# Performance work log

Measured on AMD Instinct MI355X. Metric: run time of the kernel, lower is better.

Reference implementation:

```python
import jax, jax.numpy as jnp
import numpy as np

N = 50000   # nodes
E = 800000  # edges
D = 128     # feature width (in_feats == hidden dims)
LN_EPS = 1e-5


def _degrees(src, dst, n):
    ones = jnp.ones(src.shape[0], dtype=jnp.float32)
    deg_out = jax.ops.segment_sum(ones, src, num_segments=n)
    deg_in = jax.ops.segment_sum(ones, dst, num_segments=n)
    # DGL norm='both' clamps degrees to min 1
    return jnp.maximum(deg_out, 1.0), jnp.maximum(deg_in, 1.0)


def _graph_conv(h, src, dst, inv_sqrt_out, inv_sqrt_in, W, b):
    # DGL GraphConv, norm='both': D^{-1/2} A^T D^{-1/2} X W + b
    h = h * inv_sqrt_out[:, None]                       # pre-normalize by src out-degree
    msgs = h[src]                                       # [E, D] gather
    agg = jax.ops.segment_sum(msgs, dst, num_segments=N)  # scatter-add to dst
    agg = agg * inv_sqrt_in[:, None]                    # post-normalize by dst in-degree
    return agg @ W + b


def _layer_norm(x, gamma, beta):
    mu = jnp.mean(x, axis=-1, keepdims=True)
    var = jnp.mean((x - mu) ** 2, axis=-1, keepdims=True)
    return (x - mu) * jax.lax.rsqrt(var + LN_EPS) * gamma + beta


def setup_inputs() -> dict:
    key = jax.random.key(0)
    ks = jax.random.split(key, 8)
    features = jax.random.normal(ks[0], (N, D), dtype=jnp.float32)
    src = jax.random.randint(ks[1], (E,), 0, N, dtype=jnp.int64)
    dst = jax.random.randint(ks[2], (E,), 0, N, dtype=jnp.int64)
    scale = 1.0 / np.sqrt(D)
    W1 = jax.random.normal(ks[3], (D, D), dtype=jnp.float32) * scale
    b1 = jnp.zeros((D,), dtype=jnp.float32)
    g1 = jnp.ones((D,), dtype=jnp.float32)
    be1 = jnp.zeros((D,), dtype=jnp.float32)
    W2 = jax.random.normal(ks[4], (D, D), dtype=jnp.float32) * scale
    b2 = jnp.zeros((D,), dtype=jnp.float32)
    g2 = jnp.ones((D,), dtype=jnp.float32)
    be2 = jnp.zeros((D,), dtype=jnp.float32)
    return {"features": features, "src": src, "dst": dst,
            "W1": W1, "b1": b1, "g1": g1, "be1": be1,
            "W2": W2, "b2": b2, "g2": g2, "be2": be2}


def reference(features, src, dst, W1, b1, g1, be1, W2, b2, g2, be2):
    deg_out, deg_in = _degrees(src, dst, N)
    iso = jax.lax.rsqrt(deg_out)
    isi = jax.lax.rsqrt(deg_in)
    # layer 1: GraphConv -> LayerNorm -> ReLU (dropout p=0, eval mode)
    h = _graph_conv(features, src, dst, iso, isi, W1, b1)
    h = jax.nn.relu(_layer_norm(h, g1, be1))
    # layer 2
    h = _graph_conv(h, src, dst, iso, isi, W2, b2)
    h = jax.nn.relu(_layer_norm(h, g2, be2))
    return h
```

## Files before the change

### kernel.cpp

```cpp
#include <hip/hip_runtime.h>
#include <stdint.h>

#define NN 50000
#define DD 128
#define EE 800000
#define LN_EPS 1e-5f
#define SCAN_BLOCKS ((NN + 255) / 256)
#define ROWS 16
#define ASTRIDE 136

#define CH 256
#define EC (EE / CH)
#define NP8 50000
#define NW (NP8 / 4)

typedef __attribute__((ext_vector_type(8))) short bf8_t;
typedef __attribute__((ext_vector_type(4))) float f32x4;

static __device__ __forceinline__ unsigned short f2bf(float f) {
    unsigned u = __float_as_uint(f);
    u += 0x7FFFu + ((u >> 16) & 1u);
    return (unsigned short)(u >> 16);
}

#define BF16ACC(u) do { \
    acc[0] += __uint_as_float((u).x << 16); \
    acc[1] += __uint_as_float((u).x & 0xffff0000u); \
    acc[2] += __uint_as_float((u).y << 16); \
    acc[3] += __uint_as_float((u).y & 0xffff0000u); \
    acc[4] += __uint_as_float((u).z << 16); \
    acc[5] += __uint_as_float((u).z & 0xffff0000u); \
    acc[6] += __uint_as_float((u).w << 16); \
    acc[7] += __uint_as_float((u).w & 0xffff0000u); \
} while (0)

__global__ __launch_bounds__(256) void hist_kernel(
    const int* __restrict__ src, const int* __restrict__ dst,
    unsigned char* __restrict__ epos8,
    unsigned int* __restrict__ histI, unsigned int* __restrict__ histO) {
    __shared__ unsigned int lh[NW];
    int tid = threadIdx.x;
    int c = blockIdx.x;
    int e0 = c * EC, e1 = e0 + EC;

    for (int w = tid; w < NW; w += 256) lh[w] = 0;
    __syncthreads();
    for (int e = e0 + tid; e < e1; e += 256) {
        int d = dst[e];
        int f = (d & 3) * 8;
        unsigned old = atomicAdd(&lh[d >> 2], 1u << f);
        epos8[e] = (unsigned char)(old >> f);
    }
    __syncthreads();
    {
        unsigned int* o = histI + (size_t)c * NW;
        for (int w = tid; w < NW; w += 256) o[w] = lh[w];
    }
    __syncthreads();

    for (int w = tid; w < NW; w += 256) lh[w] = 0;
    __syncthreads();
    for (int e = e0 + tid; e < e1; e += 256) {
        int d = src[e];
        atomicAdd(&lh[d >> 2], 1u << ((d & 3) * 8));
    }
    __syncthreads();
    {
        unsigned int* o = histO + (size_t)c * NW;
        for (int w = tid; w < NW; w += 256) o[w] = lh[w];
    }
}

__global__ __launch_bounds__(256) void sum_kernel(
    unsigned char* __restrict__ histI8,
    const unsigned char* __restrict__ histO8,
    int* __restrict__ cntI, float* __restrict__ iso, float* __restrict__ isi,
    int* __restrict__ bsum) {
    __shared__ int s[256];
    int tid = threadIdx.x;
    int n = blockIdx.x * 256 + tid;

    int ci = 0, co = 0;
    if (n < NN) {
#pragma unroll 8
        for (int c = 0; c < CH; c++) {
            size_t idx = (size_t)c * NP8 + n;
            unsigned char v = histI8[idx];
            histI8[idx] = (unsigned char)ci;
            ci += v;
            co += histO8[idx];
        }
        iso[n] = rsqrtf(fmaxf((float)co, 1.0f));
        isi[n] = rsqrtf(fmaxf((float)ci, 1.0f));
        cntI[n] = ci;
    }
    s[tid] = (n < NN) ? ci : 0;
    __syncthreads();
    for (int off = 128; off > 0; off >>= 1) {
        if (tid < off) s[tid] += s[tid + off];
        __syncthreads();
    }
    if (tid == 0) bsum[blockIdx.x] = s[0];
}

__global__ __launch_bounds__(256) void scanC_kernel(
    const int* __restrict__ cnt, const int* __restrict__ bsum,
    int* __restrict__ rowptr,
    const float* __restrict__ feat, const float* __restrict__ iso,
    unsigned short* __restrict__ hb) {
    __shared__ int s[256];
    __shared__ int base_s;
    __shared__ float iso_s[256];
    int tid = threadIdx.x;
    int i = blockIdx.x * 256 + tid;

    int bv = (tid < SCAN_BLOCKS && tid < blockIdx.x) ? bsum[tid] : 0;
    s[tid] = bv;
    __syncthreads();
    for (int off = 128; off > 0; off >>= 1) {
        if (tid < off) s[tid] += s[tid + off];
        __syncthreads();
    }
    if (tid == 0) base_s = s[0];
    __syncthreads();
    int base = base_s;

    iso_s[tid] = (i < NN) ? iso[i] : 1.f;
    __syncthreads();

    int v = (i < NN) ? cnt[i] : 0;
    s[tid] = v;
    __syncthreads();
    for (int off = 1; off < 256; off <<= 1) {
        int t = (tid >= off) ? s[tid - off] : 0;
        __syncthreads();
        s[tid] += t;
        __syncthreads();
    }
    if (i < NN) rowptr[i] = base + s[tid] - v;
    if (blockIdx.x == 0 && tid == 0) rowptr[NN] = EE;

    int rr = tid >> 5;
    int q = tid & 31;
    int row0 = blockIdx.x * 256;
#pragma unroll 4
    for (int it = 0; it < 32; it++) {
        int r = it * 8 + rr;
        int row = row0 + r;
        if (row < NN) {
            float sc = iso_s[r];
            float4 fv = ((const float4*)feat)[(size_t)row * 32 + q];
            ushort4 o;
            o.x = f2bf(fv.x * sc); o.y = f2bf(fv.y * sc);
            o.z = f2bf(fv.z * sc); o.w = f2bf(fv.w * sc);
            ((ushort4*)hb)[(size_t)row * 32 + q] = o;
        }
    }
}

__global__ void fill_kernel(const int* __restrict__ src, const int* __restrict__ dst,
                            const unsigned char* __restrict__ epos8,
                            const unsigned char* __restrict__ choff8,
                            const int* __restrict__ rowptr, int* __restrict__ csr,
                            const float* __restrict__ W1, const float* __restrict__ W2,
                            unsigned short* __restrict__ wbt1, unsigned short* __restrict__ wbt2) {
    int e = blockIdx.x * blockDim.x + threadIdx.x;
    if (e < EE) {
        int d = dst[e];
        int c = e / EC;
        int pos = rowptr[d] + (int)choff8[(size_t)c * NP8 + d] + (int)epos8[e];
        csr[pos] = src[e];
    }
    if (blockIdx.x < 128) {
        int idx = (blockIdx.x & 63) * 256 + threadIdx.x;
        const float* W = (blockIdx.x < 64) ? W1 : W2;
        unsigned short* wt = (blockIdx.x < 64) ? wbt1 : wbt2;
        int k = idx >> 7, n = idx & 127;
        wt[n * 128 + k] = f2bf(W[idx]);
    }
}

template <int OUTMODE>
__global__ __launch_bounds__(256) void fused_layer(
    const unsigned short* __restrict__ hb, const int* __restrict__ csr,
    const int* __restrict__ rowptr, const float* __restrict__ isi,
    const float* __restrict__ iso,
    const unsigned short* __restrict__ wbt, const float* __restrict__ b,
    const float* __restrict__ g, const float* __restrict__ be,
    float* __restrict__ outf, unsigned short* __restrict__ outb) {
    __shared__ unsigned short Asb[ROWS][ASTRIDE];
    __shared__ float redS[4][16], redSS[4][16];

    int tid = threadIdx.x;
    int node0 = blockIdx.x * ROWS;
    int w = tid >> 6;
    int lane = tid & 63;
    int quad = lane >> 4;
    int l = lane & 15;

    {
        int r = tid >> 4;
        int n = node0 + r;
        float acc[8];
#pragma unroll
        for (int i = 0; i < 8; i++) acc[i] = 0.f;
        int beg = rowptr[n];
        int end = rowptr[n + 1];
        int j = beg;
        for (; j + 7 < end; j += 8) {
            int s0 = csr[j];     int s1 = csr[j + 1];
            int s2 = csr[j + 2]; int s3 = csr[j + 3];
            int s4 = csr[j + 4]; int s5 = csr[j + 5];
            int s6 = csr[j + 6]; int s7 = csr[j + 7];
            uint4 u0 = ((const uint4*)(hb + (size_t)s0 * DD))[l];
            uint4 u1 = ((const uint4*)(hb + (size_t)s1 * DD))[l];
            uint4 u2 = ((const uint4*)(hb + (size_t)s2 * DD))[l];
            uint4 u3 = ((const uint4*)(hb + (size_t)s3 * DD))[l];
            uint4 u4 = ((const uint4*)(hb + (size_t)s4 * DD))[l];
            uint4 u5 = ((const uint4*)(hb + (size_t)s5 * DD))[l];
            uint4 u6 = ((const uint4*)(hb + (size_t)s6 * DD))[l];
            uint4 u7 = ((const uint4*)(hb + (size_t)s7 * DD))[l];
            BF16ACC(u0); BF16ACC(u1); BF16ACC(u2); BF16ACC(u3);
            BF16ACC(u4); BF16ACC(u5); BF16ACC(u6); BF16ACC(u7);
        }
        for (; j < end; j++) {
            int s0 = csr[j];
            uint4 u0 = ((const uint4*)(hb + (size_t)s0 * DD))[l];
            BF16ACC(u0);
        }
        uint4 pk;
        pk.x = (unsigned)f2bf(acc[0]) | ((unsigned)f2bf(acc[1]) << 16);
        pk.y = (unsigned)f2bf(acc[2]) | ((unsigned)f2bf(acc[3]) << 16);
        pk.z = (unsigned)f2bf(acc[4]) | ((unsigned)f2bf(acc[5]) << 16);
        pk.w = (unsigned)f2bf(acc[6]) | ((unsigned)f2bf(acc[7]) << 16);
        *(uint4*)&Asb[r][l * 8] = pk;
    }
    __syncthreads();

    bf8_t af[4];
#pragma unroll
    for (int kb = 0; kb < 4; kb++)
        af[kb] = *(bf8_t*)&Asb[l][kb * 32 + quad * 8];

    f32x4 acc[2];
#pragma unroll
    for (int tc = 0; tc < 2; tc++) acc[tc] = (f32x4){0.f, 0.f, 0.f, 0.f};

#pragma unroll
    for (int tc = 0; tc < 2; tc++) {
        int n = w * 32 + tc * 16 + l;
#pragma unroll
        for (int kb = 0; kb < 4; kb++) {
            bf8_t bfr = *(const bf8_t*)&wbt[(size_t)n * 128 + kb * 32 + quad * 8];
            acc[tc] = __builtin_amdgcn_mfma_f32_16x16x32_bf16(af[kb], bfr, acc[tc], 0, 0, 0);
        }
    }

    float bb[2], ggv[2], bev[2];
    int cbase = w * 32 + l;
#pragma unroll
    for (int tc = 0; tc < 2; tc++) {
        int c = cbase + tc * 16;
        bb[tc] = b[c]; ggv[tc] = g[c]; bev[tc] = be[c];
    }

    float s[4], ss[4];
#pragma unroll
    for (int i = 0; i < 4; i++) {
        int n = node0 + quad * 4 + i;
        float isin = isi[n];
        s[i] = 0.f; ss[i] = 0.f;
#pragma unroll
        for (int tc = 0; tc < 2; tc++) {
            float v = acc[tc][i] * isin + bb[tc];
            acc[tc][i] = v;
            s[i] += v; ss[i] += v * v;
        }
    }
#pragma unroll
    for (int i = 0; i < 4; i++) {
#pragma unroll
        for (int m = 1; m <= 8; m <<= 1) {
            s[i] += __shfl_xor(s[i], m);
            ss[i] += __shfl_xor(ss[i], m);
        }
    }
    if (l == 0) {
#pragma unroll
        for (int i = 0; i < 4; i++) {
            redS[w][quad * 4 + i] = s[i];
            redSS[w][quad * 4 + i] = ss[i];
        }
    }
    __syncthreads();

#pragma unroll
    for (int i = 0; i < 4; i++) {
        int r = quad * 4 + i;
        float S  = redS[0][r] + redS[1][r] + redS[2][r] + redS[3][r];
        float SS = redSS[0][r] + redSS[1][r] + redSS[2][r] + redSS[3][r];
        float mu = S * (1.f / 128.f);
        float var = SS * (1.f / 128.f) - mu * mu;
        float rstd = rsqrtf(var + LN_EPS);
        int n = node0 + r;
        float isov = (OUTMODE == 1) ? iso[n] : 0.f;
        size_t base = (size_t)n * DD;
#pragma unroll
        for (int tc = 0; tc < 2; tc++) {
            float o = fmaxf((acc[tc][i] - mu) * rstd * ggv[tc] + bev[tc], 0.f);
            int c = cbase + tc * 16;
            if (OUTMODE == 0) {
                outf[base + c] = o;
            } else {
                outb[base + c] = f2bf(o * isov);
            }
        }
    }
}

static inline char* alignp(char* p, size_t a) {
    return (char*)(((uintptr_t)p + a - 1) & ~(uintptr_t)(a - 1));
}

extern "C" void kernel_launch(void* const* d_in, const int* in_sizes, int n_in,
                              void* d_out, int out_size, void* d_ws, size_t ws_size,
                              hipStream_t stream) {
    const float* features = (const float*)d_in[0];
    const int*   src      = (const int*)d_in[1];
    const int*   dst      = (const int*)d_in[2];
    const float* W1  = (const float*)d_in[3];
    const float* b1  = (const float*)d_in[4];
    const float* g1  = (const float*)d_in[5];
    const float* be1 = (const float*)d_in[6];
    const float* W2  = (const float*)d_in[7];
    const float* b2  = (const float*)d_in[8];
    const float* g2  = (const float*)d_in[9];
    const float* be2 = (const float*)d_in[10];
    float* out = (float*)d_out;

    char* p = (char*)d_ws;
    int* cntI = (int*)p;                 p = alignp(p + NN * 4, 256);
    int* rowptr = (int*)p;               p = alignp(p + (NN + 1) * 4, 256);
    int* bsum = (int*)p;                 p = alignp(p + SCAN_BLOCKS * 4, 256);
    int* csr = (int*)p;                  p = alignp(p + (size_t)EE * 4, 256);
    float* iso = (float*)p;              p = alignp(p + NN * 4, 256);
    float* isi = (float*)p;              p = alignp(p + NN * 4, 256);
    unsigned short* hb1 = (unsigned short*)p;  p = alignp(p + (size_t)NN * DD * 2, 256);
    unsigned short* hb2 = (unsigned short*)p;  p = alignp(p + (size_t)NN * DD * 2, 256);
    unsigned short* wbt1 = (unsigned short*)p; p = alignp(p + DD * DD * 2, 256);
    unsigned short* wbt2 = (unsigned short*)p; p = alignp(p + DD * DD * 2, 256);
    unsigned char* epos8 = (unsigned char*)p;  p = alignp(p + EE, 256);

    unsigned char* histI8 = (unsigned char*)hb2;
    unsigned char* histO8 = (unsigned char*)hb1;

    hist_kernel<<<CH, 256, 0, stream>>>(src, dst, epos8,
                                        (unsigned int*)histI8, (unsigned int*)histO8);
    sum_kernel<<<SCAN_BLOCKS, 256, 0, stream>>>(histI8, histO8, cntI, iso, isi, bsum);
    scanC_kernel<<<SCAN_BLOCKS, 256, 0, stream>>>(cntI, bsum, rowptr, features, iso, hb1);
    fill_kernel<<<(EE + 255) / 256, 256, 0, stream>>>(src, dst, epos8, histI8,
                                                      rowptr, csr, W1, W2, wbt1, wbt2);

    const int fblocks = NN / ROWS;
    fused_layer<1><<<fblocks, 256, 0, stream>>>(hb1, csr, rowptr, isi, iso,
                                                wbt1, b1, g1, be1, nullptr, hb2);
    fused_layer<0><<<fblocks, 256, 0, stream>>>(hb2, csr, rowptr, isi, iso,
                                                wbt2, b2, g2, be2, out, nullptr);
}
```

Measured before the change: 255.3 us.

## Fuse degree histograms, recompute edge slots in fill, and predicate gather tail

The histogram kernel now builds the in-degree and out-degree shared-memory histograms in a single pass over the edges, using two LDS arrays, and no longer writes per-edge slot bytes. The fill kernel now runs one block per edge chunk. It loads that chunk's offsets into LDS and recomputes each edge's slot with LDS atomics, which removes the epos8 buffer and its global round trip. The aggregation loop in the fused layer replaces the unrolled-by-8 loop plus scalar tail with a single masked loop that clamps indices, so short rows issue duplicate loads. Risks: per-block LDS use becomes large (about 100KB in the histogram kernel), fill parallelism drops to 256 blocks, and CSR order within a row becomes nondeterministic.

After: 232.9 us. 1.1x faster.

```diff
diff --git a/kernel.cpp b/kernel.cpp
--- a/kernel.cpp
+++ b/kernel.cpp
@@ -36,38 +36,26 @@
 
 __global__ __launch_bounds__(256) void hist_kernel(
     const int* __restrict__ src, const int* __restrict__ dst,
-    unsigned char* __restrict__ epos8,
     unsigned int* __restrict__ histI, unsigned int* __restrict__ histO) {
-    __shared__ unsigned int lh[NW];
+    __shared__ unsigned int lhI[NW];
+    __shared__ unsigned int lhO[NW];
     int tid = threadIdx.x;
     int c = blockIdx.x;
     int e0 = c * EC, e1 = e0 + EC;
 
-    for (int w = tid; w < NW; w += 256) lh[w] = 0;
+    for (int w = tid; w < NW; w += 256) { lhI[w] = 0; lhO[w] = 0; }
     __syncthreads();
     for (int e = e0 + tid; e < e1; e += 256) {
         int d = dst[e];
-        int f = (d & 3) * 8;
-        unsigned old = atomicAdd(&lh[d >> 2], 1u << f);
-        epos8[e] = (unsigned char)(old >> f);
+        int s = src[e];
+        atomicAdd(&lhI[d >> 2], 1u << ((d & 3) * 8));
+        atomicAdd(&lhO[s >> 2], 1u << ((s & 3) * 8));
     }
     __syncthreads();
     {
-        unsigned int* o = histI + (size_t)c * NW;
-        for (int w = tid; w < NW; w += 256) o[w] = lh[w];
-    }
-    __syncthreads();
-
-    for (int w = tid; w < NW; w += 256) lh[w] = 0;
-    __syncthreads();
-    for (int e = e0 + tid; e < e1; e += 256) {
-        int d = src[e];
-        atomicAdd(&lh[d >> 2], 1u << ((d & 3) * 8));
-    }
-    __syncthreads();
-    {
-        unsigned int* o = histO + (size_t)c * NW;
-        for (int w = tid; w < NW; w += 256) o[w] = lh[w];
+        unsigned int* oi = histI + (size_t)c * NW;
+        unsigned int* oo = histO + (size_t)c * NW;
+        for (int w = tid; w < NW; w += 256) { oi[w] = lhI[w]; oo[w] = lhO[w]; }
     }
 }
 
@@ -158,23 +146,34 @@
     }
 }
 
-__global__ void fill_kernel(const int* __restrict__ src, const int* __restrict__ dst,
-                            const unsigned char* __restrict__ epos8,
-                            const unsigned char* __restrict__ choff8,
-                            const int* __restrict__ rowptr, int* __restrict__ csr,
-                            const float* __restrict__ W1, const float* __restrict__ W2,
-                            unsigned short* __restrict__ wbt1, unsigned short* __restrict__ wbt2) {
-    int e = blockIdx.x * blockDim.x + threadIdx.x;
-    if (e < EE) {
+__global__ __launch_bounds__(256) void fill_kernel(
+    const int* __restrict__ src, const int* __restrict__ dst,
+    const unsigned char* __restrict__ choff8,
+    const int* __restrict__ rowptr, int* __restrict__ csr,
+    const float* __restrict__ W1, const float* __restrict__ W2,
+    unsigned short* __restrict__ wbt1, unsigned short* __restrict__ wbt2) {
+    __shared__ unsigned int lh[NW];
+    __shared__ unsigned char lco[NP8];
+    int tid = threadIdx.x;
+    int c = blockIdx.x;
+    int e0 = c * EC, e1 = e0 + EC;
+
+    {
+        const unsigned int* ci = (const unsigned int*)(choff8 + (size_t)c * NP8);
+        for (int w = tid; w < NW; w += 256) { lh[w] = 0; ((unsigned int*)lco)[w] = ci[w]; }
+    }
+    __syncthreads();
+    for (int e = e0 + tid; e < e1; e += 256) {
         int d = dst[e];
-        int c = e / EC;
-        int pos = rowptr[d] + (int)choff8[(size_t)c * NP8 + d] + (int)epos8[e];
-        csr[pos] = src[e];
-    }
-    if (blockIdx.x < 128) {
-        int idx = (blockIdx.x & 63) * 256 + threadIdx.x;
-        const float* W = (blockIdx.x < 64) ? W1 : W2;
-        unsigned short* wt = (blockIdx.x < 64) ? wbt1 : wbt2;
+        int f = (d & 3) * 8;
+        unsigned old = atomicAdd(&lh[d >> 2], 1u << f);
+        int epos = (int)((old >> f) & 0xffu);
+        csr[rowptr[d] + (int)lco[d] + epos] = src[e];
+    }
+    if (c < 128) {
+        int idx = (c & 63) * 256 + tid;
+        const float* W = (c < 64) ? W1 : W2;
+        unsigned short* wt = (c < 64) ? wbt1 : wbt2;
         int k = idx >> 7, n = idx & 127;
         wt[n * 128 + k] = f2bf(W[idx]);
     }
@@ -206,27 +205,23 @@
         for (int i = 0; i < 8; i++) acc[i] = 0.f;
         int beg = rowptr[n];
         int end = rowptr[n + 1];
-        int j = beg;
-        for (; j + 7 < end; j += 8) {
-            int s0 = csr[j];     int s1 = csr[j + 1];
-            int s2 = csr[j + 2]; int s3 = csr[j + 3];
-            int s4 = csr[j + 4]; int s5 = csr[j + 5];
-            int s6 = csr[j + 6]; int s7 = csr[j + 7];
-            uint4 u0 = ((const uint4*)(hb + (size_t)s0 * DD))[l];
-            uint4 u1 = ((const uint4*)(hb + (size_t)s1 * DD))[l];
-            uint4 u2 = ((const uint4*)(hb + (size_t)s2 * DD))[l];
-            uint4 u3 = ((const uint4*)(hb + (size_t)s3 * DD))[l];
-            uint4 u4 = ((const uint4*)(hb + (size_t)s4 * DD))[l];
-            uint4 u5 = ((const uint4*)(hb + (size_t)s5 * DD))[l];
-            uint4 u6 = ((const uint4*)(hb + (size_t)s6 * DD))[l];
-            uint4 u7 = ((const uint4*)(hb + (size_t)s7 * DD))[l];
-            BF16ACC(u0); BF16ACC(u1); BF16ACC(u2); BF16ACC(u3);
-            BF16ACC(u4); BF16ACC(u5); BF16ACC(u6); BF16ACC(u7);
-        }
-        for (; j < end; j++) {
-            int s0 = csr[j];
-            uint4 u0 = ((const uint4*)(hb + (size_t)s0 * DD))[l];
-            BF16ACC(u0);
+        for (int j = beg; j < end; j += 8) {
+            uint4 u[8];
+            unsigned m[8];
+#pragma unroll
+            for (int i = 0; i < 8; i++) {
+                int t = j + i;
+                int tc = (t < end) ? t : (end - 1);
+                m[i] = (t < end) ? 0xffffffffu : 0u;
+                int s = csr[tc];
+                u[i] = ((const uint4*)(hb + (size_t)s * DD))[l];
+            }
+#pragma unroll
+            for (int i = 0; i < 8; i++) {
+                uint4 v = u[i];
+                v.x &= m[i]; v.y &= m[i]; v.z &= m[i]; v.w &= m[i];
+                BF16ACC(v);
+            }
         }
         uint4 pk;
         pk.x = (unsigned)f2bf(acc[0]) | ((unsigned)f2bf(acc[1]) << 16);
@@ -349,17 +344,16 @@
     unsigned short* hb2 = (unsigned short*)p;  p = alignp(p + (size_t)NN * DD * 2, 256);
     unsigned short* wbt1 = (unsigned short*)p; p = alignp(p + DD * DD * 2, 256);
     unsigned short* wbt2 = (unsigned short*)p; p = alignp(p + DD * DD * 2, 256);
-    unsigned char* epos8 = (unsigned char*)p;  p = alignp(p + EE, 256);
 
     unsigned char* histI8 = (unsigned char*)hb2;
     unsigned char* histO8 = (unsigned char*)hb1;
 
-    hist_kernel<<<CH, 256, 0, stream>>>(src, dst, epos8,
+    hist_kernel<<<CH, 256, 0, stream>>>(src, dst,
                                         (unsigned int*)histI8, (unsigned int*)histO8);
     sum_kernel<<<SCAN_BLOCKS, 256, 0, stream>>>(histI8, histO8, cntI, iso, isi, bsum);
     scanC_kernel<<<SCAN_BLOCKS, 256, 0, stream>>>(cntI, bsum, rowptr, features, iso, hb1);
-    fill_kernel<<<(EE + 255) / 256, 256, 0, stream>>>(src, dst, epos8, histI8,
-                                                      rowptr, csr, W1, W2, wbt1, wbt2);
+    fill_kernel<<<CH, 256, 0, stream>>>(src, dst, histI8, rowptr, csr,
+                                        W1, W2, wbt1, wbt2);
 
     const int fblocks = NN / ROWS;
     fused_layer<1><<<fblocks, 256, 0, stream>>>(hb1, csr, rowptr, isi, iso,
```
